# Optimization experiments

Measured on AMD Instinct MI355X. Metric: run time of the kernel, lower is better.

## Reference

```python
import jax, jax.numpy as jnp
import numpy as np

NUM_ITERATIONS = 3


def squash(s):
    # Faithful to the torch code: norm taken over dim=2 of (B,1,out_units,out_size,1),
    # i.e. over the out_units axis of (B, out_units, out_size).
    mag_sq = jnp.sum(s * s, axis=1, keepdims=True)  # (B,1,out_size)
    mag = jnp.sqrt(mag_sq)
    return mag_sq / (1.0 + mag_sq) * (s / mag)


def setup_inputs() -> dict:
    key = jax.random.key(0)
    k1, k2 = jax.random.split(key)
    B, in_units, in_size = 256, 8, 1152
    out_units, out_size = 10, 16
    x = jax.random.normal(k1, (B, in_units, in_size), dtype=jnp.float32)
    W = jax.random.normal(k2, (1, in_size, out_units, out_size, in_units), dtype=jnp.float32)
    return {"x": x, "W": W}


def reference(x, W):
    B = x.shape[0]
    in_size, out_units, out_size, in_units = W.shape[1:]
    Wm = W[0]  # (in_size, out_units, out_size, in_units)
    # u_hat[b,i,j,d] = sum_u W[i,j,d,u] * x[b,u,i]
    u_hat = jnp.einsum("ijdu,bui->bijd", Wm, x)  # (B, in_size, out_units, out_size)

    b_ij = jnp.ones((in_size, out_units), dtype=x.dtype)
    v = None
    for _ in range(NUM_ITERATIONS):
        c_ij = jax.nn.softmax(b_ij, axis=0)  # softmax over in_size (dim=1 in torch)
        s_j = jnp.einsum("ij,bijd->bjd", c_ij, u_hat)  # (B, out_units, out_size)
        v = squash(s_j)
        # agreement, averaged over batch as in the torch code
        u_vj1 = jnp.einsum("bijd,bjd->ij", u_hat, v) / B
        b_ij = b_ij + u_vj1
    # torch returns v_j.squeeze(1) with trailing singleton: (B, out_units, out_size, 1)
    return v[..., None]
```

## Files before the change

### kernel.cpp

```cpp
#include <hip/hip_runtime.h>
#include <cstddef>

#define BB   256
#define UU   8
#define ISZ  1152
#define JJ   10
#define DD   16
#define JD   (JJ*DD)
#define K1   (UU*ISZ)
#define ICH  16
#define NIC  (ISZ/ICH)
#define NJH  5

typedef short v8s __attribute__((ext_vector_type(8)));
typedef float f4v __attribute__((ext_vector_type(4)));
typedef unsigned short ush;

__device__ __forceinline__ ush f2bf(float f) {
    unsigned int u = __float_as_uint(f);
    unsigned int r = (u + 0x7fffu + ((u >> 16) & 1u)) >> 16;
    return (ush)r;
}
__device__ __forceinline__ float bf2f(ush h) {
    return __uint_as_float(((unsigned int)h) << 16);
}

__global__ void prep_kernel(const float* __restrict__ x,
                            ush* __restrict__ xsh, ush* __restrict__ xsl,
                            ush* __restrict__ xth, ush* __restrict__ xtl,
                            float* __restrict__ b_ij, unsigned* __restrict__ done) {
    __shared__ float buf[32][8][65];
    int it = blockIdx.x;
    int bt = blockIdx.y;
    int i0 = it * 64, b0 = bt * 32;
    int t = threadIdx.x, lane = t & 63, wv = t >> 6;

    int flat = bt * 18 + it;
    if (flat < 45) b_ij[flat * 256 + t] = 1.0f;
    if (flat == 0 && t < 16) done[t] = 0;

    for (int rep = 0; rep < 64; ++rep) {
        int row = rep * 4 + wv;
        int bl = row >> 3, u = row & 7;
        buf[bl][u][lane] = x[(size_t)(b0 + bl) * K1 + (size_t)u * ISZ + i0 + lane];
    }
    __syncthreads();
    {
        int bl = t >> 3, u = t & 7;
        for (int il = 0; il < 64; ++il) {
            float v = buf[bl][u][il];
            ush h = f2bf(v);
            size_t o = (size_t)(i0 + il) * 2048 + (size_t)(b0 + bl) * 8 + u;
            xsh[o] = h; xsl[o] = f2bf(v - bf2f(h));
        }
    }
    {
        int g = t >> 5, bl = t & 31;
        for (int pass = 0; pass < 64; ++pass) {
            int cu = pass * 8 + g;
            int u = cu >> 6, il = cu & 63;
            float v = buf[bl][u][il];
            ush h = f2bf(v);
            size_t o = (size_t)(u * ISZ + i0 + il) * BB + b0 + bl;
            xth[o] = h; xtl[o] = f2bf(v - bf2f(h));
        }
    }
}

__global__ __launch_bounds__(256, 2) void sgemm_fused(
        const ush* __restrict__ xsh, const ush* __restrict__ xsl,
        const float* __restrict__ W, const float* __restrict__ c_tab,
        float* __restrict__ s_part, int it) {
    int ic = blockIdx.x, jh = blockIdx.y;
    int j0 = jh * 2, i0 = ic * ICH;
    int t = threadIdx.x, lane = t & 63, wv = t >> 6;
    int col = lane & 15, q = lane >> 4;

    __shared__ __align__(16) ush bh_[2][16][136];
    __shared__ __align__(16) ush bl_[2][16][136];
    __shared__ float c_lds[2][ICH];

    if (t < 2 * ICH) {
        int cj = t >> 4, ci = t & 15;
        c_lds[cj][ci] = (it == 0) ? (1.0f / 1152.0f)
                                  : c_tab[(size_t)(j0 + cj) * ISZ + i0 + ci];
    }
    __syncthreads();

    for (int slot = t; slot < 512; slot += 256) {
        int jj = slot >> 8, rem = slot & 255, ii = rem >> 4, d = rem & 15;
        const float* wp = W + (size_t)(i0 + ii) * 1280 + (j0 + jj) * 128 + d * 8;
        float4 wa = *(const float4*)wp;
        float4 wb = *(const float4*)(wp + 4);
        float ci = c_lds[jj][ii];
        float vals[8] = { wa.x * ci, wa.y * ci, wa.z * ci, wa.w * ci,
                          wb.x * ci, wb.y * ci, wb.z * ci, wb.w * ci };
        v8s hv, lv;
#pragma unroll
        for (int u = 0; u < 8; ++u) {
            ush h = f2bf(vals[u]);
            hv[u] = (short)h;
            lv[u] = (short)f2bf(vals[u] - bf2f(h));
        }
        *(v8s*)&bh_[jj][d][ii * 8] = hv;
        *(v8s*)&bl_[jj][d][ii * 8] = lv;
    }
    __syncthreads();

    int m_base = wv * 64;
    f4v acc[4][2];
#pragma unroll
    for (int mm = 0; mm < 4; ++mm)
#pragma unroll
        for (int jj = 0; jj < 2; ++jj) acc[mm][jj] = (f4v){0.f, 0.f, 0.f, 0.f};

#pragma unroll
    for (int s = 0; s < 4; ++s) {
        v8s bh0 = *(const v8s*)&bh_[0][col][s * 32 + q * 8];
        v8s bl0 = *(const v8s*)&bl_[0][col][s * 32 + q * 8];
        v8s bh1 = *(const v8s*)&bh_[1][col][s * 32 + q * 8];
        v8s bl1 = *(const v8s*)&bl_[1][col][s * 32 + q * 8];
        size_t abase = (size_t)(i0 + s * 4 + q) * 2048;
#pragma unroll
        for (int mm = 0; mm < 4; ++mm) {
            size_t ao = abase + (size_t)(m_base + mm * 16 + col) * 8;
            v8s ah = *(const v8s*)(xsh + ao);
            v8s al = *(const v8s*)(xsl + ao);
            acc[mm][0] = __builtin_amdgcn_mfma_f32_16x16x32_bf16(ah, bh0, acc[mm][0], 0, 0, 0);
            acc[mm][0] = __builtin_amdgcn_mfma_f32_16x16x32_bf16(ah, bl0, acc[mm][0], 0, 0, 0);
            acc[mm][0] = __builtin_amdgcn_mfma_f32_16x16x32_bf16(al, bh0, acc[mm][0], 0, 0, 0);
            acc[mm][1] = __builtin_amdgcn_mfma_f32_16x16x32_bf16(ah, bh1, acc[mm][1], 0, 0, 0);
            acc[mm][1] = __builtin_amdgcn_mfma_f32_16x16x32_bf16(ah, bl1, acc[mm][1], 0, 0, 0);
            acc[mm][1] = __builtin_amdgcn_mfma_f32_16x16x32_bf16(al, bh1, acc[mm][1], 0, 0, 0);
        }
    }
#pragma unroll
    for (int mm = 0; mm < 4; ++mm)
#pragma unroll
        for (int jj = 0; jj < 2; ++jj)
#pragma unroll
            for (int r = 0; r < 4; ++r)
                s_part[((size_t)(m_base + mm * 16 + q * 4 + r) * NIC + ic) * JD
                       + (j0 + jj) * DD + col] = acc[mm][jj][r];
}

__global__ void reduce_squash(const float* __restrict__ s_part, float* __restrict__ v,
                              ush* __restrict__ vth, ush* __restrict__ vtl) {
    int b = blockIdx.x, t = threadIdx.x;
    __shared__ float sm[JD];
    if (t < JD) {
        const float* sp = s_part + (size_t)b * NIC * JD + t;
        float s = 0.f;
#pragma unroll 8
        for (int p = 0; p < NIC; ++p) s += sp[(size_t)p * JD];
        sm[t] = s;
    }
    __syncthreads();
    if (t < JD) {
        int d = t & 15;
        float msq = 0.f;
#pragma unroll
        for (int j = 0; j < JJ; ++j) { float xx = sm[j * DD + d]; msq += xx * xx; }
        float val = msq / (1.f + msq) * sm[t] * rsqrtf(msq);
        v[(size_t)b * JD + t] = val;
        ush h = f2bf(val);
        vth[(size_t)t * BB + b] = h;
        vtl[(size_t)t * BB + b] = f2bf(val - bf2f(h));
    }
}

__global__ __launch_bounds__(256) void mgemm_agree(
        const ush* __restrict__ Ah, const ush* __restrict__ Al,
        const ush* __restrict__ Bh, const ush* __restrict__ Bl,
        const float* __restrict__ W, float* __restrict__ b_ij,
        float* __restrict__ c_tab, unsigned* __restrict__ done, int it) {
    int wv = threadIdx.x >> 6, lane = threadIdx.x & 63;
    int col = lane & 15, q = lane >> 4;
    int w = blockIdx.x * 4 + wv;
    int mt = w / 288, nt2 = w % 288;
    int m0 = mt * 16;
#pragma unroll
    for (int rep = 0; rep < 2; ++rep) {
        int nt = nt2 * 2 + rep;
        int n0 = nt * 16;
        size_t aoff = (size_t)(m0 + col) * BB + q * 8;
        size_t boff = (size_t)(n0 + col) * BB + q * 8;
        f4v acc = {0.f, 0.f, 0.f, 0.f};
#pragma unroll
        for (int s = 0; s < BB / 32; ++s) {
            v8s ah = *(const v8s*)(Ah + aoff);
            v8s al = *(const v8s*)(Al + aoff);
            v8s bh = *(const v8s*)(Bh + boff);
            v8s bl = *(const v8s*)(Bl + boff);
            acc = __builtin_amdgcn_mfma_f32_16x16x32_bf16(ah, bh, acc, 0, 0, 0);
            acc = __builtin_amdgcn_mfma_f32_16x16x32_bf16(ah, bl, acc, 0, 0, 0);
            acc = __builtin_amdgcn_mfma_f32_16x16x32_bf16(al, bh, acc, 0, 0, 0);
            aoff += 32; boff += 32;
        }
        int u = nt / 72;
        int i = (nt % 72) * 16 + col;
        const float* Wp = W + (size_t)i * 1280 + mt * 128 + q * 32 + u;
        float p = Wp[0] * acc[0] + Wp[8] * acc[1] + Wp[16] * acc[2] + Wp[24] * acc[3];
        p += __shfl_xor(p, 16, 64);
        p += __shfl_xor(p, 32, 64);
        if (q == 0) atomicAdd(&b_ij[(size_t)mt * ISZ + i], p * (1.0f / 256.0f));
    }

    __shared__ unsigned lastf;
    asm volatile("s_waitcnt vmcnt(0)" ::: "memory");
    __syncthreads();
    if (threadIdx.x == 0) {
        unsigned old = __hip_atomic_fetch_add(&done[it], 1u,
                           __ATOMIC_RELAXED, __HIP_MEMORY_SCOPE_AGENT);
        lastf = (old == 719u);
    }
    __syncthreads();
    if (lastf) {
        for (int j = wv; j < JJ; j += 4) {
            const float* bp = b_ij + (size_t)j * ISZ;
            float vals[18];
#pragma unroll
            for (int k = 0; k < 18; ++k) vals[k] = bp[lane + 64 * k];
            float m = -1e30f;
#pragma unroll
            for (int k = 0; k < 18; ++k) m = fmaxf(m, vals[k]);
#pragma unroll
            for (int off = 32; off; off >>= 1) m = fmaxf(m, __shfl_xor(m, off, 64));
            float ssum = 0.f;
#pragma unroll
            for (int k = 0; k < 18; ++k) ssum += __expf(vals[k] - m);
#pragma unroll
            for (int off = 32; off; off >>= 1) ssum += __shfl_xor(ssum, off, 64);
            float inv = 1.f / ssum;
#pragma unroll
            for (int k = 0; k < 18; ++k)
                c_tab[(size_t)j * ISZ + lane + 64 * k] = __expf(vals[k] - m) * inv;
        }
    }
}

extern "C" void kernel_launch(void* const* d_in, const int* in_sizes, int n_in,
                              void* d_out, int out_size, void* d_ws, size_t ws_size,
                              hipStream_t stream) {
    const float* x = (const float*)d_in[0];
    const float* W = (const float*)d_in[1];
    float* v_out = (float*)d_out;

    float* b_ij  = (float*)d_ws;
    float* c_tab = b_ij + ISZ * JJ;
    float* dptr  = c_tab + ISZ * JJ;
    unsigned* done = (unsigned*)dptr;
    float* s_part = dptr + 64;
    ush* xsh = (ush*)(s_part + (size_t)BB * NIC * JD);
    ush* xsl = xsh + (size_t)ISZ * 2048;
    ush* xth = xsl + (size_t)ISZ * 2048;
    ush* xtl = xth + (size_t)K1 * BB;
    ush* vth = xtl + (size_t)K1 * BB;
    ush* vtl = vth + (size_t)JD * BB;

    hipLaunchKernelGGL(prep_kernel, dim3(18, 8), dim3(256), 0, stream,
                       x, xsh, xsl, xth, xtl, b_ij, done);
    for (int it = 0; it < 3; ++it) {
        hipLaunchKernelGGL(sgemm_fused, dim3(NIC, NJH), dim3(256), 0, stream,
                           xsh, xsl, W, c_tab, s_part, it);
        hipLaunchKernelGGL(reduce_squash, dim3(BB), dim3(192), 0, stream,
                           s_part, v_out, vth, vtl);
        if (it < 2) {
            hipLaunchKernelGGL(mgemm_agree, dim3(720), dim3(256), 0, stream,
                               vth, vtl, xth, xtl, W, b_ij, c_tab, done, it);
        }
    }
}
```

Measured before the change: 180.7 us.

## Fuse squash reduction into sgemm via in-kernel hierarchical grid barrier

Merges the reduce_squash kernel into the sgemm kernel. All 360 blocks signal completion through a two-level atomic counter tree, and the first 256 blocks spin on per-group go flags before each reduces one batch row of partial sums. The partial-sum stores and loads use cache-bypassing (sc0 sc1) instructions for cross-block visibility, and the sync counters move to a memset region. This removes three kernel launches and their gaps, but risks deadlock if not all 360 blocks are co-resident, and adds spin-wait overhead.

After: 182.6 us. About the same (+1.1%).

```diff
diff --git a/kernel.cpp b/kernel.cpp
--- a/kernel.cpp
+++ b/kernel.cpp
@@ -12,6 +12,14 @@
 #define NIC  (ISZ/ICH)
 #define NJH  5
 
+#define L_ARR(it,c)  ((it)*18 + (c))
+#define L_L2(it)     (54 + (it))
+#define L_GO(it,g)   (57 + (it)*36 + (g))
+#define L_MD(it)     (165 + (it))
+#define SYNC_LINES   168
+#define SYNC_U32     (SYNC_LINES*64)
+#define SYNC_BYTES   (SYNC_U32*4)
+
 typedef short v8s __attribute__((ext_vector_type(8)));
 typedef float f4v __attribute__((ext_vector_type(4)));
 typedef unsigned short ush;
@@ -24,11 +32,17 @@
 __device__ __forceinline__ float bf2f(ush h) {
     return __uint_as_float(((unsigned int)h) << 16);
 }
+__device__ __forceinline__ void st_dword_sc1(float* p, float v) {
+    asm volatile("global_store_dword %0, %1, off sc0 sc1" :: "v"(p), "v"(v) : "memory");
+}
+__device__ __forceinline__ unsigned llc_add(unsigned* p) {
+    return __hip_atomic_fetch_add(p, 1u, __ATOMIC_RELAXED, __HIP_MEMORY_SCOPE_AGENT);
+}
 
 __global__ void prep_kernel(const float* __restrict__ x,
                             ush* __restrict__ xsh, ush* __restrict__ xsl,
                             ush* __restrict__ xth, ush* __restrict__ xtl,
-                            float* __restrict__ b_ij, unsigned* __restrict__ done) {
+                            float* __restrict__ b_ij) {
     __shared__ float buf[32][8][65];
     int it = blockIdx.x;
     int bt = blockIdx.y;
@@ -37,7 +51,6 @@
 
     int flat = bt * 18 + it;
     if (flat < 45) b_ij[flat * 256 + t] = 1.0f;
-    if (flat == 0 && t < 16) done[t] = 0;
 
     for (int rep = 0; rep < 64; ++rep) {
         int row = rep * 4 + wv;
@@ -67,11 +80,14 @@
     }
 }
 
-__global__ __launch_bounds__(256, 2) void sgemm_fused(
+__global__ __launch_bounds__(256, 2) void sgemm_red(
         const ush* __restrict__ xsh, const ush* __restrict__ xsl,
         const float* __restrict__ W, const float* __restrict__ c_tab,
-        float* __restrict__ s_part, int it) {
+        float* __restrict__ s_part, float* __restrict__ v_out,
+        ush* __restrict__ vth, ush* __restrict__ vtl,
+        unsigned* __restrict__ sync, int it) {
     int ic = blockIdx.x, jh = blockIdx.y;
+    int fb = jh * NIC + ic;
     int j0 = jh * 2, i0 = ic * ICH;
     int t = threadIdx.x, lane = t & 63, wv = t >> 6;
     int col = lane & 15, q = lane >> 4;
@@ -79,6 +95,7 @@
     __shared__ __align__(16) ush bh_[2][16][136];
     __shared__ __align__(16) ush bl_[2][16][136];
     __shared__ float c_lds[2][ICH];
+    __shared__ float smr[JD];
 
     if (t < 2 * ICH) {
         int cj = t >> 4, ci = t & 15;
@@ -140,32 +157,65 @@
         for (int jj = 0; jj < 2; ++jj)
 #pragma unroll
             for (int r = 0; r < 4; ++r)
-                s_part[((size_t)(m_base + mm * 16 + q * 4 + r) * NIC + ic) * JD
-                       + (j0 + jj) * DD + col] = acc[mm][jj][r];
-}
-
-__global__ void reduce_squash(const float* __restrict__ s_part, float* __restrict__ v,
-                              ush* __restrict__ vth, ush* __restrict__ vtl) {
-    int b = blockIdx.x, t = threadIdx.x;
-    __shared__ float sm[JD];
+                st_dword_sc1(&s_part[((size_t)(m_base + mm * 16 + q * 4 + r) * NIC + ic) * JD
+                                     + (j0 + jj) * DD + col], acc[mm][jj][r]);
+
+    asm volatile("s_waitcnt vmcnt(0)" ::: "memory");
+    __syncthreads();
+    if (t == 0) {
+        unsigned old = llc_add(&sync[L_ARR(it, fb % 18) * 64]);
+        if (old == 19) {
+            unsigned o2 = llc_add(&sync[L_L2(it) * 64]);
+            if (o2 == 17) {
+                for (int g = 0; g < 36; ++g)
+                    __hip_atomic_store(&sync[L_GO(it, g) * 64], 1u,
+                                       __ATOMIC_RELAXED, __HIP_MEMORY_SCOPE_AGENT);
+            }
+        }
+    }
+    if (fb >= BB) return;
+
+    if (t == 0) {
+        while (__hip_atomic_load(&sync[L_GO(it, fb % 36) * 64], __ATOMIC_RELAXED,
+                                 __HIP_MEMORY_SCOPE_AGENT) == 0u) {
+            __builtin_amdgcn_s_sleep(32);
+        }
+    }
+    __syncthreads();
+
+    int b = fb;
     if (t < JD) {
-        const float* sp = s_part + (size_t)b * NIC * JD + t;
+        const float* sp0 = s_part + (size_t)b * NIC * JD + t;
         float s = 0.f;
-#pragma unroll 8
-        for (int p = 0; p < NIC; ++p) s += sp[(size_t)p * JD];
-        sm[t] = s;
+        float tmp[12];
+#pragma unroll
+        for (int c = 0; c < 6; ++c) {
+#pragma unroll
+            for (int u = 0; u < 12; ++u)
+                asm volatile("global_load_dword %0, %1, off sc0 sc1"
+                             : "=v"(tmp[u])
+                             : "v"(sp0 + (size_t)(c * 12 + u) * JD));
+            asm volatile("s_waitcnt vmcnt(0)" ::: "memory");
+            __builtin_amdgcn_sched_barrier(0);
+#pragma unroll
+            for (int u = 0; u < 12; ++u) s += tmp[u];
+        }
+        smr[t] = s;
     }
     __syncthreads();
     if (t < JD) {
         int d = t & 15;
         float msq = 0.f;
 #pragma unroll
-        for (int j = 0; j < JJ; ++j) { float xx = sm[j * DD + d]; msq += xx * xx; }
-        float val = msq / (1.f + msq) * sm[t] * rsqrtf(msq);
-        v[(size_t)b * JD + t] = val;
-        ush h = f2bf(val);
-        vth[(size_t)t * BB + b] = h;
-        vtl[(size_t)t * BB + b] = f2bf(val - bf2f(h));
+        for (int j = 0; j < JJ; ++j) { float xx = smr[j * DD + d]; msq += xx * xx; }
+        float val = msq / (1.f + msq) * smr[t] * rsqrtf(msq);
+        if (it == 2) {
+            v_out[(size_t)b * JD + t] = val;
+        } else {
+            ush h = f2bf(val);
+            vth[(size_t)t * BB + b] = h;
+            vtl[(size_t)t * BB + b] = f2bf(val - bf2f(h));
+        }
     }
 }
 
@@ -173,7 +223,7 @@
         const ush* __restrict__ Ah, const ush* __restrict__ Al,
         const ush* __restrict__ Bh, const ush* __restrict__ Bl,
         const float* __restrict__ W, float* __restrict__ b_ij,
-        float* __restrict__ c_tab, unsigned* __restrict__ done, int it) {
+        float* __restrict__ c_tab, unsigned* __restrict__ sync, int it) {
     int wv = threadIdx.x >> 6, lane = threadIdx.x & 63;
     int col = lane & 15, q = lane >> 4;
     int w = blockIdx.x * 4 + wv;
@@ -210,8 +260,7 @@
     asm volatile("s_waitcnt vmcnt(0)" ::: "memory");
     __syncthreads();
     if (threadIdx.x == 0) {
-        unsigned old = __hip_atomic_fetch_add(&done[it], 1u,
-                           __ATOMIC_RELAXED, __HIP_MEMORY_SCOPE_AGENT);
+        unsigned old = llc_add(&sync[L_MD(it) * 64]);
         lastf = (old == 719u);
     }
     __syncthreads();
@@ -246,11 +295,10 @@
     const float* W = (const float*)d_in[1];
     float* v_out = (float*)d_out;
 
-    float* b_ij  = (float*)d_ws;
+    unsigned* sync = (unsigned*)d_ws;
+    float* b_ij  = (float*)d_ws + SYNC_U32;
     float* c_tab = b_ij + ISZ * JJ;
-    float* dptr  = c_tab + ISZ * JJ;
-    unsigned* done = (unsigned*)dptr;
-    float* s_part = dptr + 64;
+    float* s_part = c_tab + ISZ * JJ;
     ush* xsh = (ush*)(s_part + (size_t)BB * NIC * JD);
     ush* xsl = xsh + (size_t)ISZ * 2048;
     ush* xth = xsl + (size_t)ISZ * 2048;
@@ -258,16 +306,15 @@
     ush* vth = xtl + (size_t)K1 * BB;
     ush* vtl = vth + (size_t)JD * BB;
 
+    hipMemsetAsync(d_ws, 0, SYNC_BYTES, stream);
     hipLaunchKernelGGL(prep_kernel, dim3(18, 8), dim3(256), 0, stream,
-                       x, xsh, xsl, xth, xtl, b_ij, done);
+                       x, xsh, xsl, xth, xtl, b_ij);
     for (int it = 0; it < 3; ++it) {
-        hipLaunchKernelGGL(sgemm_fused, dim3(NIC, NJH), dim3(256), 0, stream,
-                           xsh, xsl, W, c_tab, s_part, it);
-        hipLaunchKernelGGL(reduce_squash, dim3(BB), dim3(192), 0, stream,
-                           s_part, v_out, vth, vtl);
+        hipLaunchKernelGGL(sgemm_red, dim3(NIC, NJH), dim3(256), 0, stream,
+                           xsh, xsl, W, c_tab, s_part, v_out, vth, vtl, sync, it);
         if (it < 2) {
             hipLaunchKernelGGL(mgemm_agree, dim3(720), dim3(256), 0, stream,
-                               vth, vtl, xth, xtl, W, b_ij, c_tab, done, it);
-        }
-    }
-}
+                               vth, vtl, xth, xtl, W, b_ij, c_tab, sync, it);
+        }
+    }
+}
```
